# Kernel tuning notes

Measured on AMD Instinct MI355X. Metric: run time of the kernel, lower is better.

## Reference

```python
import jax, jax.numpy as jnp
import numpy as np

N = 50000        # nodes
E = 800000       # random edges (self loops appended inside reference, per PyG default)
IN = 128         # in_channels
H1, C1 = 8, 64   # conv1: heads, hidden_channels
NUM_CLASSES = 2  # conv2 out (heads=1, concat=False)
NEG_SLOPE = 0.2  # PyG GATConv default LeakyReLU slope


def setup_inputs() -> dict:
    key = jax.random.key(0)
    ks = jax.random.split(key, 12)
    x = jax.random.normal(ks[0], (N, IN), dtype=jnp.float32)
    edge_index = jax.random.randint(ks[1], (2, E), 0, N)
    # conv1 params: W1 [IN, H1*C1], att vectors [H1, C1], bias [H1*C1]
    W1 = jax.random.normal(ks[2], (IN, H1 * C1), dtype=jnp.float32) / np.sqrt(IN)
    a_src1 = jax.random.normal(ks[3], (H1, C1), dtype=jnp.float32) / np.sqrt(C1)
    a_dst1 = jax.random.normal(ks[4], (H1, C1), dtype=jnp.float32) / np.sqrt(C1)
    b1 = jnp.zeros((H1 * C1,), dtype=jnp.float32)
    # conv2 params: heads=1, out=NUM_CLASSES
    W2 = jax.random.normal(ks[5], (H1 * C1, 1 * NUM_CLASSES), dtype=jnp.float32) / np.sqrt(H1 * C1)
    a_src2 = jax.random.normal(ks[6], (1, NUM_CLASSES), dtype=jnp.float32) / np.sqrt(NUM_CLASSES)
    a_dst2 = jax.random.normal(ks[7], (1, NUM_CLASSES), dtype=jnp.float32) / np.sqrt(NUM_CLASSES)
    b2 = jnp.zeros((NUM_CLASSES,), dtype=jnp.float32)
    return {"x": x, "edge_index": edge_index, "W1": W1, "a_src1": a_src1,
            "a_dst1": a_dst1, "b1": b1, "W2": W2, "a_src2": a_src2,
            "a_dst2": a_dst2, "b2": b2}


def gat_layer(x, src, dst, W, a_src, a_dst, bias, concat):
    n = x.shape[0]
    heads, ch = a_src.shape
    h = (x @ W).reshape(n, heads, ch)                      # [N,H,C]
    alpha_s = jnp.einsum('nhc,hc->nh', h, a_src)           # per-node src score
    alpha_d = jnp.einsum('nhc,hc->nh', h, a_dst)           # per-node dst score
    e = jax.nn.leaky_relu(alpha_s[src] + alpha_d[dst], NEG_SLOPE)  # [Etot,H]
    # segment softmax over edges grouped by destination node
    m = jax.ops.segment_max(e, dst, num_segments=n)
    ex = jnp.exp(e - m[dst])
    den = jax.ops.segment_sum(ex, dst, num_segments=n)
    alpha = ex / den[dst]                                  # [Etot,H]
    out = jax.ops.segment_sum(h[src] * alpha[:, :, None], dst, num_segments=n)  # [N,H,C]
    out = out.reshape(n, heads * ch) if concat else out.mean(axis=1)
    return out + bias


def reference(x, edge_index, W1, a_src1, a_dst1, b1, W2, a_src2, a_dst2, b2):
    n = x.shape[0]
    loops = jnp.arange(n, dtype=edge_index.dtype)
    src = jnp.concatenate([edge_index[0], loops])   # PyG add_self_loops=True
    dst = jnp.concatenate([edge_index[1], loops])
    h = gat_layer(x, src, dst, W1, a_src1, a_dst1, b1, concat=True)   # [N, H1*C1]
    h = jax.nn.elu(h)
    # dropout is identity in eval mode
    out = gat_layer(h, src, dst, W2, a_src2, a_dst2, b2, concat=False)  # [N, 2]
    return out
```

## Files before the change

kernel.cpp:

```cpp
#include <hip/hip_runtime.h>
#include <hip/hip_bf16.h>

#define NEG 0.2f
#define BKT 64

typedef __attribute__((ext_vector_type(8))) short bf16x8;
typedef __attribute__((ext_vector_type(4))) float f32x4;

static __device__ __forceinline__ unsigned short f2bf(float f) {
    union { float f; unsigned u; } v; v.f = f;
    unsigned r = v.u + 0x7fff + ((v.u >> 16) & 1);
    return (unsigned short)(r >> 16);
}
static __device__ __forceinline__ float bf_lo(unsigned u) {
    return __uint_as_float(u << 16);
}
static __device__ __forceinline__ float bf_hi(unsigned u) {
    return __uint_as_float(u & 0xffff0000u);
}

__global__ void k_init(int* __restrict__ deg, unsigned short* __restrict__ csr, int n) {
    int v = blockIdx.x * 256 + threadIdx.x;
    if (v >= n) return;
    deg[v] = 1;
    csr[(size_t)v * BKT] = (unsigned short)v;
}

__global__ __launch_bounds__(256) void k_big(const int* __restrict__ ei,
                                             int* __restrict__ deg,
                                             unsigned short* __restrict__ csr,
                                             const float* __restrict__ x,
                                             const float* __restrict__ W1,
                                             const float* __restrict__ a_src,
                                             const float* __restrict__ a_dst,
                                             unsigned short* __restrict__ h1b,
                                             float* __restrict__ as1,
                                             float* __restrict__ ad1,
                                             int E_, int n, int gblocks) {
    int tid = threadIdx.x;
    if ((int)blockIdx.x >= gblocks) {
        int e = (blockIdx.x - gblocks) * 256 + tid;
        if (e >= E_) return;
        int s = ei[e], d = ei[E_ + e];
        int slot = atomicAdd(&deg[d], 1);
        if (slot < BKT) csr[(size_t)d * BKT + slot] = (unsigned short)s;
        return;
    }
    __shared__ unsigned short stg[4][16][72];
    int wave = tid >> 6, lane = tid & 63;
    int l15 = lane & 15, q = lane >> 4;
    int rowblk = blockIdx.x * 256 + wave * 64;

    bf16x8 xf[4][4];
    #pragma unroll
    for (int st = 0; st < 4; st++) {
        int ar = rowblk + st * 16 + l15; if (ar > n - 1) ar = n - 1;
        const float* ap = x + (size_t)ar * 128 + q * 8;
        #pragma unroll
        for (int kb = 0; kb < 4; kb++) {
            float4 v0 = *(const float4*)(ap + kb * 32);
            float4 v1 = *(const float4*)(ap + kb * 32 + 4);
            xf[st][kb][0] = (short)f2bf(v0.x); xf[st][kb][1] = (short)f2bf(v0.y);
            xf[st][kb][2] = (short)f2bf(v0.z); xf[st][kb][3] = (short)f2bf(v0.w);
            xf[st][kb][4] = (short)f2bf(v1.x); xf[st][kb][5] = (short)f2bf(v1.y);
            xf[st][kb][6] = (short)f2bf(v1.z); xf[st][kb][7] = (short)f2bf(v1.w);
        }
    }

    for (int j = 0; j < 8; j++) {
        int col0 = j * 64;
        bf16x8 bfr[4][4];
        #pragma unroll
        for (int kb = 0; kb < 4; kb++)
            #pragma unroll
            for (int t = 0; t < 4; t++) {
                const float* wp = W1 + (size_t)(kb * 32 + q * 8) * 512 + col0 + t * 16 + l15;
                #pragma unroll
                for (int e = 0; e < 8; e++)
                    bfr[kb][t][e] = (short)f2bf(wp[(size_t)e * 512]);
            }
        float asv[4], adv[4];
        #pragma unroll
        for (int t = 0; t < 4; t++) {
            asv[t] = a_src[j * 64 + t * 16 + l15];
            adv[t] = a_dst[j * 64 + t * 16 + l15];
        }

        #pragma unroll
        for (int st = 0; st < 4; st++) {
            int row0 = rowblk + st * 16;
            f32x4 acc[4] = {};
            #pragma unroll
            for (int kb = 0; kb < 4; kb++)
                #pragma unroll
                for (int t = 0; t < 4; t++)
                    acc[t] = __builtin_amdgcn_mfma_f32_16x16x32_bf16(xf[st][kb], bfr[kb][t], acc[t], 0, 0, 0);
            #pragma unroll
            for (int t = 0; t < 4; t++)
                #pragma unroll
                for (int r = 0; r < 4; r++)
                    stg[wave][q * 4 + r][t * 16 + l15] = f2bf(acc[t][r]);
            #pragma unroll
            for (int p = 0; p < 2; p++) {
                int lr = p * 8 + (lane >> 3);
                int row = row0 + lr;
                int cd = (lane & 7) * 8;
                uint4 vv = *(const uint4*)&stg[wave][lr][cd];
                if (row < n)
                    *(uint4*)(h1b + (size_t)row * 512 + col0 + cd) = vv;
            }
            float ps[4], pd[4];
            #pragma unroll
            for (int r = 0; r < 4; r++) {
                ps[r] = acc[0][r] * asv[0] + acc[1][r] * asv[1]
                      + acc[2][r] * asv[2] + acc[3][r] * asv[3];
                pd[r] = acc[0][r] * adv[0] + acc[1][r] * adv[1]
                      + acc[2][r] * adv[2] + acc[3][r] * adv[3];
                #pragma unroll
                for (int off = 1; off < 16; off <<= 1) {
                    ps[r] += __shfl_xor(ps[r], off, 64);
                    pd[r] += __shfl_xor(pd[r], off, 64);
                }
            }
            if (l15 < 4) {
                int r = l15;
                float vps = ps[0], vpd = pd[0];
                if (r == 1) { vps = ps[1]; vpd = pd[1]; }
                if (r == 2) { vps = ps[2]; vpd = pd[2]; }
                if (r == 3) { vps = ps[3]; vpd = pd[3]; }
                int row = row0 + q * 4 + r;
                if (row < n) { as1[row * 8 + j] = vps; ad1[row * 8 + j] = vpd; }
            }
        }
    }
}

__global__ __launch_bounds__(256) void k_agg1(const unsigned short* __restrict__ h1b,
                                              const float* __restrict__ as1,
                                              const float* __restrict__ ad1,
                                              const float* __restrict__ b1,
                                              const float* __restrict__ W2,
                                              const int* __restrict__ deg,
                                              const unsigned short* __restrict__ csr,
                                              float* __restrict__ h2, int n) {
    int lane = threadIdx.x & 63;
    int v = blockIdx.x * 4 + (threadIdx.x >> 6);
    if (v >= n) return;
    int head = lane >> 3, c = lane * 8;
    int dv = deg[v]; if (dv > BKT) dv = BKT;
    const unsigned short* cp = csr + (size_t)v * BKT;
    float adh = ad1[v * 8 + head];
    float s = 0.f;
    float acc[8] = {};
    int i = 0;
    for (; i + 4 <= dv; i += 4) {
        ushort4 uu = *(const ushort4*)(cp + i);
        int u0 = uu.x, u1 = uu.y, u2 = uu.z, u3 = uu.w;
        float ea = as1[u0 * 8 + head] + adh;
        float eb = as1[u1 * 8 + head] + adh;
        float ec = as1[u2 * 8 + head] + adh;
        float ed = as1[u3 * 8 + head] + adh;
        uint4 h0 = *(const uint4*)(h1b + (size_t)u0 * 512 + c);
        uint4 h1 = *(const uint4*)(h1b + (size_t)u1 * 512 + c);
        uint4 h2v = *(const uint4*)(h1b + (size_t)u2 * 512 + c);
        uint4 h3 = *(const uint4*)(h1b + (size_t)u3 * 512 + c);
        ea = (ea >= 0.f) ? ea : NEG * ea;
        eb = (eb >= 0.f) ? eb : NEG * eb;
        ec = (ec >= 0.f) ? ec : NEG * ec;
        ed = (ed >= 0.f) ? ed : NEG * ed;
        float w0 = __expf(ea), w1 = __expf(eb), w2 = __expf(ec), w3 = __expf(ed);
        s += (w0 + w1) + (w2 + w3);
        acc[0] = fmaf(w3, bf_lo(h3.x), fmaf(w2, bf_lo(h2v.x), fmaf(w1, bf_lo(h1.x), fmaf(w0, bf_lo(h0.x), acc[0]))));
        acc[1] = fmaf(w3, bf_hi(h3.x), fmaf(w2, bf_hi(h2v.x), fmaf(w1, bf_hi(h1.x), fmaf(w0, bf_hi(h0.x), acc[1]))));
        acc[2] = fmaf(w3, bf_lo(h3.y), fmaf(w2, bf_lo(h2v.y), fmaf(w1, bf_lo(h1.y), fmaf(w0, bf_lo(h0.y), acc[2]))));
        acc[3] = fmaf(w3, bf_hi(h3.y), fmaf(w2, bf_hi(h2v.y), fmaf(w1, bf_hi(h1.y), fmaf(w0, bf_hi(h0.y), acc[3]))));
        acc[4] = fmaf(w3, bf_lo(h3.z), fmaf(w2, bf_lo(h2v.z), fmaf(w1, bf_lo(h1.z), fmaf(w0, bf_lo(h0.z), acc[4]))));
        acc[5] = fmaf(w3, bf_hi(h3.z), fmaf(w2, bf_hi(h2v.z), fmaf(w1, bf_hi(h1.z), fmaf(w0, bf_hi(h0.z), acc[5]))));
        acc[6] = fmaf(w3, bf_lo(h3.w), fmaf(w2, bf_lo(h2v.w), fmaf(w1, bf_lo(h1.w), fmaf(w0, bf_lo(h0.w), acc[6]))));
        acc[7] = fmaf(w3, bf_hi(h3.w), fmaf(w2, bf_hi(h2v.w), fmaf(w1, bf_hi(h1.w), fmaf(w0, bf_hi(h0.w), acc[7]))));
    }
    for (; i < dv; i++) {
        int u = cp[i];
        float e = as1[u * 8 + head] + adh;
        e = (e >= 0.f) ? e : NEG * e;
        float w = __expf(e);
        s += w;
        uint4 hv = *(const uint4*)(h1b + (size_t)u * 512 + c);
        acc[0] = fmaf(w, bf_lo(hv.x), acc[0]);
        acc[1] = fmaf(w, bf_hi(hv.x), acc[1]);
        acc[2] = fmaf(w, bf_lo(hv.y), acc[2]);
        acc[3] = fmaf(w, bf_hi(hv.y), acc[3]);
        acc[4] = fmaf(w, bf_lo(hv.z), acc[4]);
        acc[5] = fmaf(w, bf_hi(hv.z), acc[5]);
        acc[6] = fmaf(w, bf_lo(hv.w), acc[6]);
        acc[7] = fmaf(w, bf_hi(hv.w), acc[7]);
    }
    float inv = 1.0f / s;
    float4 ba = *(const float4*)(b1 + c);
    float4 bb = *(const float4*)(b1 + c + 4);
    float o[8] = {acc[0] * inv + ba.x, acc[1] * inv + ba.y,
                  acc[2] * inv + ba.z, acc[3] * inv + ba.w,
                  acc[4] * inv + bb.x, acc[5] * inv + bb.y,
                  acc[6] * inv + bb.z, acc[7] * inv + bb.w};
    #pragma unroll
    for (int jj = 0; jj < 8; jj++)
        o[jj] = (o[jj] > 0.f) ? o[jj] : (__expf(o[jj]) - 1.0f);
    const float4* wp = (const float4*)(W2 + c * 2);
    float4 w0 = wp[0], w1 = wp[1], w2 = wp[2], w3 = wp[3];
    float p0 = o[0] * w0.x + o[1] * w0.z + o[2] * w1.x + o[3] * w1.z
             + o[4] * w2.x + o[5] * w2.z + o[6] * w3.x + o[7] * w3.z;
    float p1 = o[0] * w0.y + o[1] * w0.w + o[2] * w1.y + o[3] * w1.w
             + o[4] * w2.y + o[5] * w2.w + o[6] * w3.y + o[7] * w3.w;
    #pragma unroll
    for (int off = 1; off < 64; off <<= 1) {
        p0 += __shfl_xor(p0, off, 64);
        p1 += __shfl_xor(p1, off, 64);
    }
    if (lane == 0) {
        h2[2 * v] = p0;
        h2[2 * v + 1] = p1;
    }
}

__global__ __launch_bounds__(256) void k_agg2(const float* __restrict__ h2,
                                              const float* __restrict__ a_src2,
                                              const float* __restrict__ a_dst2,
                                              const float* __restrict__ b2,
                                              const int* __restrict__ deg,
                                              const unsigned short* __restrict__ csr,
                                              float* __restrict__ out, int n) {
    int tid = threadIdx.x;
    int lane = tid & 63, wave = tid >> 6;
    int sub = lane & 7, g = lane >> 3;
    int v = blockIdx.x * 32 + wave * 8 + g;
    if (v >= n) return;
    int dv = deg[v]; if (dv > BKT) dv = BKT;
    const unsigned short* cp = csr + (size_t)v * BKT;
    float sa0 = a_src2[0], sa1 = a_src2[1];
    float da0 = a_dst2[0], da1 = a_dst2[1];
    float2 hv = *(const float2*)(h2 + 2 * v);
    float adv = hv.x * da0 + hv.y * da1;
    float s = 0.f, a0 = 0.f, a1 = 0.f;
    for (int i = sub; i < dv; i += 8) {
        int u = cp[i];
        float2 hu = *(const float2*)(h2 + 2 * u);
        float e = hu.x * sa0 + hu.y * sa1 + adv;
        e = (e >= 0.f) ? e : NEG * e;
        float w = __expf(e);
        s += w;
        a0 = fmaf(w, hu.x, a0);
        a1 = fmaf(w, hu.y, a1);
    }
    #pragma unroll
    for (int off = 1; off < 8; off <<= 1) {
        s  += __shfl_xor(s, off, 64);
        a0 += __shfl_xor(a0, off, 64);
        a1 += __shfl_xor(a1, off, 64);
    }
    if (sub == 0) {
        float inv = 1.0f / s;
        out[2 * v]     = a0 * inv + b2[0];
        out[2 * v + 1] = a1 * inv + b2[1];
    }
}

extern "C" void kernel_launch(void* const* d_in, const int* in_sizes, int n_in,
                              void* d_out, int out_size, void* d_ws, size_t ws_size,
                              hipStream_t stream) {
    const float* x      = (const float*)d_in[0];
    const int*   ei     = (const int*)d_in[1];
    const float* W1     = (const float*)d_in[2];
    const float* a_src1 = (const float*)d_in[3];
    const float* a_dst1 = (const float*)d_in[4];
    const float* b1     = (const float*)d_in[5];
    const float* W2     = (const float*)d_in[6];
    const float* a_src2 = (const float*)d_in[7];
    const float* a_dst2 = (const float*)d_in[8];
    const float* b2     = (const float*)d_in[9];
    float* out = (float*)d_out;

    int n  = in_sizes[0] / 128;
    int E_ = in_sizes[1] / 2;
    int rblk = (n + 255) / 256;
    int npad = rblk * 256;

    char* w = (char*)d_ws;
    auto alloc = [&](size_t bytes) {
        char* p = w; w += (bytes + 255) & ~(size_t)255; return p;
    };
    int*            deg    = (int*)alloc((size_t)n * 4);
    unsigned short* csr    = (unsigned short*)alloc((size_t)n * BKT * 2);
    unsigned short* h1b    = (unsigned short*)alloc((size_t)npad * 512 * 2);
    float*          as1    = (float*)alloc((size_t)n * 8 * 4);
    float*          ad1    = (float*)alloc((size_t)n * 8 * 4);
    float*          h2     = (float*)alloc((size_t)n * 2 * 4);

    int nb256 = (n + 255) / 256;
    k_init<<<nb256, 256, 0, stream>>>(deg, csr, n);

    int gblocks = rblk;
    int sblocks = (E_ + 255) / 256;
    k_big<<<gblocks + sblocks, 256, 0, stream>>>(ei, deg, csr, x, W1,
                                                 a_src1, a_dst1, h1b, as1, ad1,
                                                 E_, n, gblocks);

    int nb = (n + 3) / 4;
    k_agg1<<<nb, 256, 0, stream>>>(h1b, as1, ad1, b1, W2, deg, csr, h2, n);

    int ab = (n + 31) / 32;
    k_agg2<<<ab, 256, 0, stream>>>(h2, a_src2, a_dst2, b2, deg, csr, out, n);
}
```

Baseline: 287.9 us.

## Slice h1 features per XCD for L2-local gather in layer-1 aggregation

h1 and the attention scores are stored head-major, split into 16 column slices of 32 bf16 each. Layer-1 aggregation is partitioned so each block handles one slice, with the block-to-slice mapping keyed on blockIdx&7 so that each XCD's L2 only ever sees a 1/8 working set of the gathered features. Per-slice partial W2 projections go to a new buffer and a new reduction kernel sums them. This adds a launch, partial-sum traffic, and 16x re-reading of the CSR and degree arrays, and it drops the 4-way unrolled gather loop.

```diff
diff --git a/kernel.cpp b/kernel.cpp
--- a/kernel.cpp
+++ b/kernel.cpp
@@ -106,8 +106,9 @@
                 int row = row0 + lr;
                 int cd = (lane & 7) * 8;
                 uint4 vv = *(const uint4*)&stg[wave][lr][cd];
+                int slice = 2 * j + (cd >> 5);
                 if (row < n)
-                    *(uint4*)(h1b + (size_t)row * 512 + col0 + cd) = vv;
+                    *(uint4*)(h1b + ((size_t)slice * n + row) * 32 + (cd & 31)) = vv;
             }
             float ps[4], pd[4];
             #pragma unroll
@@ -129,7 +130,10 @@
                 if (r == 2) { vps = ps[2]; vpd = pd[2]; }
                 if (r == 3) { vps = ps[3]; vpd = pd[3]; }
                 int row = row0 + q * 4 + r;
-                if (row < n) { as1[row * 8 + j] = vps; ad1[row * 8 + j] = vpd; }
+                if (row < n) {
+                    as1[(size_t)j * n + row] = vps;
+                    ad1[(size_t)j * n + row] = vpd;
+                }
             }
         }
     }
@@ -142,50 +146,43 @@
                                               const float* __restrict__ W2,
                                               const int* __restrict__ deg,
                                               const unsigned short* __restrict__ csr,
-                                              float* __restrict__ h2, int n) {
-    int lane = threadIdx.x & 63;
-    int v = blockIdx.x * 4 + (threadIdx.x >> 6);
-    if (v >= n) return;
-    int head = lane >> 3, c = lane * 8;
-    int dv = deg[v]; if (dv > BKT) dv = BKT;
+                                              float* __restrict__ part,
+                                              int n, int bpp) {
+    int b = blockIdx.x;
+    int xcd = b & 7;
+    int t = b >> 3;
+    int sp = (t >= bpp) ? 1 : 0;
+    int j = t - sp * bpp;
+    int slice = xcd + 8 * sp;
+    int head = slice >> 1;
+
+    int tid = threadIdx.x;
+    int lane = tid & 63, wave = tid >> 6;
+    int g = lane >> 2, sub = lane & 3;
+    int v = j * 64 + wave * 16 + g;
+    bool act = v < n;
+
+    const unsigned short* hs = h1b + (size_t)slice * n * 32 + sub * 8;
+    const float* as1h = as1 + (size_t)head * n;
+
+    float adh = 0.f;
+    int dv = 0;
+    if (act) {
+        adh = ad1[(size_t)head * n + v];
+        dv = __builtin_nontemporal_load(deg + v);
+        if (dv > BKT) dv = BKT;
+    }
     const unsigned short* cp = csr + (size_t)v * BKT;
-    float adh = ad1[v * 8 + head];
+
     float s = 0.f;
     float acc[8] = {};
-    int i = 0;
-    for (; i + 4 <= dv; i += 4) {
-        ushort4 uu = *(const ushort4*)(cp + i);
-        int u0 = uu.x, u1 = uu.y, u2 = uu.z, u3 = uu.w;
-        float ea = as1[u0 * 8 + head] + adh;
-        float eb = as1[u1 * 8 + head] + adh;
-        float ec = as1[u2 * 8 + head] + adh;
-        float ed = as1[u3 * 8 + head] + adh;
-        uint4 h0 = *(const uint4*)(h1b + (size_t)u0 * 512 + c);
-        uint4 h1 = *(const uint4*)(h1b + (size_t)u1 * 512 + c);
-        uint4 h2v = *(const uint4*)(h1b + (size_t)u2 * 512 + c);
-        uint4 h3 = *(const uint4*)(h1b + (size_t)u3 * 512 + c);
-        ea = (ea >= 0.f) ? ea : NEG * ea;
-        eb = (eb >= 0.f) ? eb : NEG * eb;
-        ec = (ec >= 0.f) ? ec : NEG * ec;
-        ed = (ed >= 0.f) ? ed : NEG * ed;
-        float w0 = __expf(ea), w1 = __expf(eb), w2 = __expf(ec), w3 = __expf(ed);
-        s += (w0 + w1) + (w2 + w3);
-        acc[0] = fmaf(w3, bf_lo(h3.x), fmaf(w2, bf_lo(h2v.x), fmaf(w1, bf_lo(h1.x), fmaf(w0, bf_lo(h0.x), acc[0]))));
-        acc[1] = fmaf(w3, bf_hi(h3.x), fmaf(w2, bf_hi(h2v.x), fmaf(w1, bf_hi(h1.x), fmaf(w0, bf_hi(h0.x), acc[1]))));
-        acc[2] = fmaf(w3, bf_lo(h3.y), fmaf(w2, bf_lo(h2v.y), fmaf(w1, bf_lo(h1.y), fmaf(w0, bf_lo(h0.y), acc[2]))));
-        acc[3] = fmaf(w3, bf_hi(h3.y), fmaf(w2, bf_hi(h2v.y), fmaf(w1, bf_hi(h1.y), fmaf(w0, bf_hi(h0.y), acc[3]))));
-        acc[4] = fmaf(w3, bf_lo(h3.z), fmaf(w2, bf_lo(h2v.z), fmaf(w1, bf_lo(h1.z), fmaf(w0, bf_lo(h0.z), acc[4]))));
-        acc[5] = fmaf(w3, bf_hi(h3.z), fmaf(w2, bf_hi(h2v.z), fmaf(w1, bf_hi(h1.z), fmaf(w0, bf_hi(h0.z), acc[5]))));
-        acc[6] = fmaf(w3, bf_lo(h3.w), fmaf(w2, bf_lo(h2v.w), fmaf(w1, bf_lo(h1.w), fmaf(w0, bf_lo(h0.w), acc[6]))));
-        acc[7] = fmaf(w3, bf_hi(h3.w), fmaf(w2, bf_hi(h2v.w), fmaf(w1, bf_hi(h1.w), fmaf(w0, bf_hi(h0.w), acc[7]))));
-    }
-    for (; i < dv; i++) {
-        int u = cp[i];
-        float e = as1[u * 8 + head] + adh;
+    for (int i = 0; i < dv; i++) {
+        int u = __builtin_nontemporal_load(cp + i);
+        float e = as1h[u] + adh;
         e = (e >= 0.f) ? e : NEG * e;
         float w = __expf(e);
         s += w;
-        uint4 hv = *(const uint4*)(h1b + (size_t)u * 512 + c);
+        uint4 hv = *(const uint4*)(hs + (size_t)u * 32);
         acc[0] = fmaf(w, bf_lo(hv.x), acc[0]);
         acc[1] = fmaf(w, bf_hi(hv.x), acc[1]);
         acc[2] = fmaf(w, bf_lo(hv.y), acc[2]);
@@ -195,31 +192,37 @@
         acc[6] = fmaf(w, bf_lo(hv.w), acc[6]);
         acc[7] = fmaf(w, bf_hi(hv.w), acc[7]);
     }
+
     float inv = 1.0f / s;
-    float4 ba = *(const float4*)(b1 + c);
-    float4 bb = *(const float4*)(b1 + c + 4);
-    float o[8] = {acc[0] * inv + ba.x, acc[1] * inv + ba.y,
-                  acc[2] * inv + ba.z, acc[3] * inv + ba.w,
-                  acc[4] * inv + bb.x, acc[5] * inv + bb.y,
-                  acc[6] * inv + bb.z, acc[7] * inv + bb.w};
+    int cbase = slice * 32 + sub * 8;
+    float p0 = 0.f, p1 = 0.f;
     #pragma unroll
-    for (int jj = 0; jj < 8; jj++)
-        o[jj] = (o[jj] > 0.f) ? o[jj] : (__expf(o[jj]) - 1.0f);
-    const float4* wp = (const float4*)(W2 + c * 2);
-    float4 w0 = wp[0], w1 = wp[1], w2 = wp[2], w3 = wp[3];
-    float p0 = o[0] * w0.x + o[1] * w0.z + o[2] * w1.x + o[3] * w1.z
-             + o[4] * w2.x + o[5] * w2.z + o[6] * w3.x + o[7] * w3.z;
-    float p1 = o[0] * w0.y + o[1] * w0.w + o[2] * w1.y + o[3] * w1.w
-             + o[4] * w2.y + o[5] * w2.w + o[6] * w3.y + o[7] * w3.w;
+    for (int k2 = 0; k2 < 8; k2++) {
+        float o = acc[k2] * inv + b1[cbase + k2];
+        o = (o > 0.f) ? o : (__expf(o) - 1.0f);
+        p0 = fmaf(o, W2[(cbase + k2) * 2], p0);
+        p1 = fmaf(o, W2[(cbase + k2) * 2 + 1], p1);
+    }
+    p0 += __shfl_xor(p0, 1, 64); p0 += __shfl_xor(p0, 2, 64);
+    p1 += __shfl_xor(p1, 1, 64); p1 += __shfl_xor(p1, 2, 64);
+    if (act && sub == 0) {
+        float* pp = part + ((size_t)slice * n + v) * 2;
+        __builtin_nontemporal_store(p0, pp);
+        __builtin_nontemporal_store(p1, pp + 1);
+    }
+}
+
+__global__ void k_red(const float* __restrict__ part, float* __restrict__ h2, int n) {
+    int v = blockIdx.x * 256 + threadIdx.x;
+    if (v >= n) return;
+    float s0 = 0.f, s1 = 0.f;
     #pragma unroll
-    for (int off = 1; off < 64; off <<= 1) {
-        p0 += __shfl_xor(p0, off, 64);
-        p1 += __shfl_xor(p1, off, 64);
-    }
-    if (lane == 0) {
-        h2[2 * v] = p0;
-        h2[2 * v + 1] = p1;
-    }
+    for (int p = 0; p < 16; p++) {
+        float2 pv = *(const float2*)(part + ((size_t)p * n + v) * 2);
+        s0 += pv.x; s1 += pv.y;
+    }
+    h2[2 * v] = s0;
+    h2[2 * v + 1] = s1;
 }
 
 __global__ __launch_bounds__(256) void k_agg2(const float* __restrict__ h2,
@@ -282,7 +285,6 @@
     int n  = in_sizes[0] / 128;
     int E_ = in_sizes[1] / 2;
     int rblk = (n + 255) / 256;
-    int npad = rblk * 256;
 
     char* w = (char*)d_ws;
     auto alloc = [&](size_t bytes) {
@@ -290,9 +292,10 @@
     };
     int*            deg    = (int*)alloc((size_t)n * 4);
     unsigned short* csr    = (unsigned short*)alloc((size_t)n * BKT * 2);
-    unsigned short* h1b    = (unsigned short*)alloc((size_t)npad * 512 * 2);
+    unsigned short* h1b    = (unsigned short*)alloc((size_t)n * 16 * 32 * 2);
     float*          as1    = (float*)alloc((size_t)n * 8 * 4);
     float*          ad1    = (float*)alloc((size_t)n * 8 * 4);
+    float*          part   = (float*)alloc((size_t)n * 16 * 2 * 4);
     float*          h2     = (float*)alloc((size_t)n * 2 * 4);
 
     int nb256 = (n + 255) / 256;
@@ -304,8 +307,11 @@
                                                  a_src1, a_dst1, h1b, as1, ad1,
                                                  E_, n, gblocks);
 
-    int nb = (n + 3) / 4;
-    k_agg1<<<nb, 256, 0, stream>>>(h1b, as1, ad1, b1, W2, deg, csr, h2, n);
+    int bpp = (n + 63) / 64;
+    k_agg1<<<16 * bpp, 256, 0, stream>>>(h1b, as1, ad1, b1, W2, deg, csr,
+                                         part, n, bpp);
+
+    k_red<<<nb256, 256, 0, stream>>>(part, h2, n);
 
     int ab = (n + 31) / 32;
     k_agg2<<<ab, 256, 0, stream>>>(h2, a_src2, a_dst2, b2, deg, csr, out, n);
```

Result: slower. 539.1 us (+87.2%).
